# Kernel tuning notes

Measured on AMD Instinct MI355X. Metric: run time of the kernel, lower is better.

## Reference

```python
import jax, jax.numpy as jnp
import numpy as np

_EPS = 1e-10
_SHIFT = 1


def setup_inputs() -> dict:
    key = jax.random.key(0)
    k1, k2 = jax.random.split(key)
    n_rays, n_samples = 262144, 128
    alpha = jax.random.uniform(k1, (n_rays, n_samples), dtype=jnp.float32)
    rgbs = jax.random.uniform(k2, (n_rays, n_samples, 3), dtype=jnp.float32)
    return {"alpha": alpha, "rgbs": rgbs}


def reference(alpha, rgbs):
    # trans[..., i] = prod_{j<=i} (1 - alpha_j + eps), then shifted right by _SHIFT
    trans = jnp.cumprod(1.0 - alpha + _EPS, axis=-1)
    trans = jnp.roll(trans, shift=_SHIFT, axis=-1)
    trans = trans.at[..., :_SHIFT].set(1.0)
    weights = trans * alpha                              # [R, S]
    rgbs_rendered = jnp.sum(weights[..., None] * rgbs, axis=-2)  # [R, 3]
    return rgbs_rendered, weights
```

## Files before the change

### kernel.cpp

```cpp
#include <hip/hip_runtime.h>

#define VR_EPS 1e-10f
#define VR_S 128

__global__ __launch_bounds__(256) void vr_kernel(
    const float* __restrict__ alpha,
    const float* __restrict__ rgbs,
    float* __restrict__ out_rgb,
    float* __restrict__ out_w,
    int n_rays)
{
    const int wave_id = (blockIdx.x * blockDim.x + threadIdx.x) >> 6;
    const int lane    = threadIdx.x & 63;
    if (wave_id >= n_rays) return;
    const size_t ray = (size_t)wave_id;

    const float2 a2 = *(const float2*)(alpha + ray * VR_S + 2 * lane);
    const float t0 = 1.0f - a2.x + VR_EPS;
    const float t1 = 1.0f - a2.y + VR_EPS;
    const float p  = t0 * t1;

    float inc = p;
    #pragma unroll
    for (int off = 1; off < 64; off <<= 1) {
        float up = __shfl_up(inc, off, 64);
        inc *= (lane >= off) ? up : 1.0f;
    }
    float exc = __shfl_up(inc, 1, 64);
    if (lane == 0) exc = 1.0f;

    const float w0 = exc * a2.x;
    const float w1 = exc * t0 * a2.y;

    *(float2*)(out_w + ray * VR_S + 2 * lane) = make_float2(w0, w1);

    const float* rp = rgbs + ray * (VR_S * 3) + 6 * lane;
    const float2 c01 = *(const float2*)(rp);
    const float2 c23 = *(const float2*)(rp + 2);
    const float2 c45 = *(const float2*)(rp + 4);

    float r = w0 * c01.x + w1 * c23.y;
    float g = w0 * c01.y + w1 * c45.x;
    float b = w0 * c23.x + w1 * c45.y;

    #pragma unroll
    for (int off = 32; off > 0; off >>= 1) {
        r += __shfl_down(r, off, 64);
        g += __shfl_down(g, off, 64);
        b += __shfl_down(b, off, 64);
    }
    if (lane == 0) {
        float* op = out_rgb + ray * 3;
        op[0] = r; op[1] = g; op[2] = b;
    }
}

extern "C" void kernel_launch(void* const* d_in, const int* in_sizes, int n_in,
                              void* d_out, int out_size, void* d_ws, size_t ws_size,
                              hipStream_t stream) {
    const float* alpha = (const float*)d_in[0];
    const float* rgbs  = (const float*)d_in[1];
    const int n_rays = in_sizes[0] / VR_S;

    float* out_rgb = (float*)d_out;
    float* out_w   = (float*)d_out + (size_t)n_rays * 3;

    const int blocks = (n_rays + 3) / 4;
    vr_kernel<<<blocks, 256, 0, stream>>>(alpha, rgbs, out_rgb, out_w, n_rays);
}
```

Baseline: 618.8 us.

## Process each ray with 16 lanes of 8 samples using float4 loads

```diff
diff --git a/kernel.cpp b/kernel.cpp
--- a/kernel.cpp
+++ b/kernel.cpp
@@ -2,6 +2,8 @@
 
 #define VR_EPS 1e-10f
 #define VR_S 128
+#define SPL 8
+#define LPR 16
 
 __global__ __launch_bounds__(256) void vr_kernel(
     const float* __restrict__ alpha,
@@ -10,47 +12,71 @@
     float* __restrict__ out_w,
     int n_rays)
 {
-    const int wave_id = (blockIdx.x * blockDim.x + threadIdx.x) >> 6;
-    const int lane    = threadIdx.x & 63;
-    if (wave_id >= n_rays) return;
-    const size_t ray = (size_t)wave_id;
+    const int tid  = blockIdx.x * blockDim.x + threadIdx.x;
+    const int lane = threadIdx.x & 63;
+    const int seg  = lane & (LPR - 1);
+    const int ray  = tid >> 4;
+    if (ray >= n_rays) return;
 
-    const float2 a2 = *(const float2*)(alpha + ray * VR_S + 2 * lane);
-    const float t0 = 1.0f - a2.x + VR_EPS;
-    const float t1 = 1.0f - a2.y + VR_EPS;
-    const float p  = t0 * t1;
+    const size_t abase = (size_t)ray * VR_S + seg * SPL;
+    const float4 a0 = *(const float4*)(alpha + abase);
+    const float4 a1 = *(const float4*)(alpha + abase + 4);
 
-    float inc = p;
+    float a[SPL] = {a0.x, a0.y, a0.z, a0.w, a1.x, a1.y, a1.z, a1.w};
+    float t[SPL];
     #pragma unroll
-    for (int off = 1; off < 64; off <<= 1) {
+    for (int i = 0; i < SPL; ++i) t[i] = 1.0f - a[i] + VR_EPS;
+
+    float P = t[0];
+    #pragma unroll
+    for (int i = 1; i < SPL; ++i) P *= t[i];
+
+    float inc = P;
+    #pragma unroll
+    for (int off = 1; off < LPR; off <<= 1) {
         float up = __shfl_up(inc, off, 64);
-        inc *= (lane >= off) ? up : 1.0f;
+        inc *= (seg >= off) ? up : 1.0f;
     }
     float exc = __shfl_up(inc, 1, 64);
-    if (lane == 0) exc = 1.0f;
+    if (seg == 0) exc = 1.0f;
 
-    const float w0 = exc * a2.x;
-    const float w1 = exc * t0 * a2.y;
+    float pre[SPL];
+    pre[0] = exc;
+    #pragma unroll
+    for (int i = 1; i < SPL; ++i) pre[i] = pre[i - 1] * t[i - 1];
 
-    *(float2*)(out_w + ray * VR_S + 2 * lane) = make_float2(w0, w1);
+    float w[SPL];
+    #pragma unroll
+    for (int i = 0; i < SPL; ++i) w[i] = pre[i] * a[i];
 
-    const float* rp = rgbs + ray * (VR_S * 3) + 6 * lane;
-    const float2 c01 = *(const float2*)(rp);
-    const float2 c23 = *(const float2*)(rp + 2);
-    const float2 c45 = *(const float2*)(rp + 4);
+    *(float4*)(out_w + abase)     = make_float4(w[0], w[1], w[2], w[3]);
+    *(float4*)(out_w + abase + 4) = make_float4(w[4], w[5], w[6], w[7]);
 
-    float r = w0 * c01.x + w1 * c23.y;
-    float g = w0 * c01.y + w1 * c45.x;
-    float b = w0 * c23.x + w1 * c45.y;
+    const float* rp = rgbs + (size_t)ray * (VR_S * 3) + seg * (SPL * 3);
+    float cf[SPL * 3];
+    #pragma unroll
+    for (int i = 0; i < 6; ++i) {
+        const float4 v = *(const float4*)(rp + 4 * i);
+        cf[4 * i + 0] = v.x; cf[4 * i + 1] = v.y;
+        cf[4 * i + 2] = v.z; cf[4 * i + 3] = v.w;
+    }
+
+    float r = 0.f, g = 0.f, b = 0.f;
+    #pragma unroll
+    for (int i = 0; i < SPL; ++i) {
+        r += w[i] * cf[3 * i + 0];
+        g += w[i] * cf[3 * i + 1];
+        b += w[i] * cf[3 * i + 2];
+    }
 
     #pragma unroll
-    for (int off = 32; off > 0; off >>= 1) {
-        r += __shfl_down(r, off, 64);
-        g += __shfl_down(g, off, 64);
-        b += __shfl_down(b, off, 64);
+    for (int off = 8; off >= 1; off >>= 1) {
+        r += __shfl_xor(r, off, 64);
+        g += __shfl_xor(g, off, 64);
+        b += __shfl_xor(b, off, 64);
     }
-    if (lane == 0) {
-        float* op = out_rgb + ray * 3;
+    if (seg == 0) {
+        float* op = out_rgb + (size_t)ray * 3;
         op[0] = r; op[1] = g; op[2] = b;
     }
 }
@@ -65,6 +91,7 @@
     float* out_rgb = (float*)d_out;
     float* out_w   = (float*)d_out + (size_t)n_rays * 3;
 
-    const int blocks = (n_rays + 3) / 4;
+    const long long total_threads = (long long)n_rays * LPR;
+    const int blocks = (int)((total_threads + 255) / 256);
     vr_kernel<<<blocks, 256, 0, stream>>>(alpha, rgbs, out_rgb, out_w, n_rays);
 }
```

New measurement: 619.3 us. Within noise of the previous version (+0.1%).
